# Kernel tuning notes

Hardware: AMD Instinct MI355X
Metric: run time of the kernel (lower is better)

The kernel has to match this reference:

```python
import jax, jax.numpy as jnp
import numpy as np

P = 2048  # number of problems


def _structure():
    # Symbols per problem alternate 128/384; questions per problem alternate 32/96.
    p = np.arange(P)
    S = np.where(p % 2 == 0, 128, 384).astype(np.int64)   # num_symbols per problem
    Q = np.where(p % 2 == 0, 32, 96).astype(np.int64)     # num_questions per problem
    cost_starts = np.concatenate([[0], np.cumsum(S)])[:-1]  # row starts into costs_flat
    prob_of_question = np.repeat(p, Q)                     # [T_Q] problem id of each question
    S_per_q = np.repeat(S, Q)                              # [T_Q] symbols per question
    TQ = S_per_q.shape[0]
    qs_segment = np.repeat(np.arange(TQ), S_per_q)         # [T_total] question id of each element
    q_elem_starts = np.concatenate([[0], np.cumsum(S_per_q)])[:-1]
    T = qs_segment.shape[0]
    # offset of each element within its question, then add that problem's cost row start
    offsets = np.arange(T) - np.repeat(q_elem_starts, S_per_q)
    starts_per_q = np.repeat(cost_starts, Q)
    cost_index = np.repeat(starts_per_q, S_per_q) + offsets  # tile_like gather indices
    return (cost_index.astype(np.int32), qs_segment.astype(np.int32),
            prob_of_question.astype(np.int32))


def setup_inputs() -> dict:
    key = jax.random.key(0)
    k1, k2, k3 = jax.random.split(key, 3)
    cost_index, qs_segment, prob_of_question = _structure()
    T = cost_index.shape[0]            # 41_943_040
    TS = (P // 2) * (128 + 384)        # 524_288
    occ_flat = jax.random.uniform(k1, (T,), dtype=jnp.float32)   # occurrence counts >= 0
    costs_flat = jax.random.normal(k2, (TS,), dtype=jnp.float32)  # symbol costs (weights)
    valid = jax.random.uniform(k3, (P,)) < 0.9                    # per-problem valid mask
    return {
        'occ_flat': occ_flat,
        'costs_flat': costs_flat,
        'valid': valid,
        'cost_index': jnp.asarray(cost_index),
        'qs_segment': jnp.asarray(qs_segment),
        'prob_of_question': jnp.asarray(prob_of_question),
    }


def reference(occ_flat, costs_flat, valid, cost_index, qs_segment, prob_of_question):
    # tile_like: broadcast each problem's costs to each of its questions (gather)
    # costs_to_logits: elementwise multiply + per-question reduce_sum
    # costs_decorated_to_logits: invalid problems' logits are 0 (scatter_nd into zeros)
    TQ = prob_of_question.shape[0]
    potentials = occ_flat * costs_flat[cost_index]             # [T_total]
    logits_q = jax.ops.segment_sum(potentials, qs_segment, num_segments=TQ)  # [T_Q]
    return jnp.where(valid[prob_of_question], logits_q, jnp.zeros((), logits_q.dtype))
```

## Files before the change

kernel.cpp:

```cpp
#include <hip/hip_runtime.h>


typedef float f4 __attribute__((ext_vector_type(4)));

__device__ __forceinline__ float dot4(f4 a, f4 b) {
    return a.x * b.x + a.y * b.y + a.z * b.z + a.w * b.w;
}

__device__ __forceinline__ float hw_reduce(float s) {
    #pragma unroll
    for (int off = 16; off > 0; off >>= 1) s += __shfl_down(s, off, 32);
    return s;
}

__global__ __launch_bounds__(256)
void classifier_kernel(const float* __restrict__ occ,
                       const float* __restrict__ costs,
                       const void*  __restrict__ valid,
                       float* __restrict__ out) {
    __shared__ f4 lds_c[256];
    const int tid   = threadIdx.x;
    const int lane  = tid & 31;
    const int hw    = tid >> 5;
    const int flane = tid & 63;

    unsigned int wdet = ((const unsigned int*)valid)[flane];
    const bool u8 = (__ballot(wdet > 1u) != 0ull);

    const int g     = blockIdx.x;
    const int group = g / 9;
    const int r     = g - group * 9;

    const f4* occ4  = (const f4*)occ;
    const f4* cost4 = (const f4*)costs;

    if (r < 8) {
        const int pair  = 2 * group + (r & 1);
        const int chunk = r >> 1;
        const int prob  = 2 * pair + 1;
        if (tid < 96) lds_c[tid] = cost4[128 * pair + 32 + tid];
        __syncthreads();
        const bool v = u8 ? (((const unsigned char*)valid)[prob] != 0)
                          : (((const int*)valid)[prob] != 0);
        const int j0 = 24 * chunk + 3 * hw;
        float s0 = 0.0f, s1 = 0.0f, s2 = 0.0f;
        if (v) {
            f4 cb0 = lds_c[lane];
            f4 cb1 = lds_c[lane + 32];
            f4 cb2 = lds_c[lane + 64];
            const f4* ob = occ4 + 10240 * pair + 1024 + 96 * j0 + lane;
            f4 a0 = __builtin_nontemporal_load(ob);
            f4 a1 = __builtin_nontemporal_load(ob + 32);
            f4 a2 = __builtin_nontemporal_load(ob + 64);
            f4 b0 = __builtin_nontemporal_load(ob + 96);
            f4 b1 = __builtin_nontemporal_load(ob + 128);
            f4 b2 = __builtin_nontemporal_load(ob + 160);
            f4 c0 = __builtin_nontemporal_load(ob + 192);
            f4 c1 = __builtin_nontemporal_load(ob + 224);
            f4 c2 = __builtin_nontemporal_load(ob + 256);
            s0 = dot4(a0, cb0) + dot4(a1, cb1) + dot4(a2, cb2);
            s1 = dot4(b0, cb0) + dot4(b1, cb1) + dot4(b2, cb2);
            s2 = dot4(c0, cb0) + dot4(c1, cb1) + dot4(c2, cb2);
        }
        s0 = hw_reduce(s0);
        s1 = hw_reduce(s1);
        s2 = hw_reduce(s2);
        if (lane == 0) {
            float* o = out + 128 * pair + 32 + j0;
            o[0] = s0; o[1] = s1; o[2] = s2;
        }
    } else {
        const int e  = group;
        const int pa = 2 * e, pb = 2 * e + 1;
        lds_c[tid] = (tid < 128) ? cost4[128 * pa + tid]
                                 : cost4[128 * pb + (tid - 128)];
        __syncthreads();
        const int p    = (hw < 4) ? pa : pb;
        const int prob = 2 * p;
        const bool v = u8 ? (((const unsigned char*)valid)[prob] != 0)
                          : (((const int*)valid)[prob] != 0);
        const int j0 = (hw & 3) * 8;
        float s[8];
        #pragma unroll
        for (int i = 0; i < 8; ++i) s[i] = 0.0f;
        if (v) {
            f4 cb = lds_c[((hw < 4) ? 0 : 128) + lane];
            const f4* ob = occ4 + 10240 * p + 32 * j0 + lane;
            #pragma unroll
            for (int i = 0; i < 8; ++i) {
                f4 a = __builtin_nontemporal_load(ob + 32 * i);
                s[i] = dot4(a, cb);
            }
        }
        #pragma unroll
        for (int i = 0; i < 8; ++i) {
            float sr = hw_reduce(s[i]);
            if (lane == 0) out[128 * p + j0 + i] = sr;
        }
    }
}

extern "C" void kernel_launch(void* const* d_in, const int* in_sizes, int n_in,
                              void* d_out, int out_size, void* d_ws, size_t ws_size,
                              hipStream_t stream) {
    const float* occ   = (const float*)d_in[0];
    const float* costs = (const float*)d_in[1];
    const void*  valid = (const void*)d_in[2];

    (void)out_size;
    const int grid  = 512 * 9;
    const int block = 256;

    classifier_kernel<<<grid, block, 0, stream>>>(occ, costs, valid, (float*)d_out);
}
```

Measured before the change: 348.0 us.

## Stream large-problem occ rows via global_load_lds with full-wave reductions

In the 384-symbol branch, the occurrence data is now staged into LDS with asynchronous global_load_lds copies, and partial vmcnt waits let compute start before all loads have landed. Each wave processes six questions as three pairs, using a 64-lane layout and full-wave shuffle reductions instead of half-wave ones. Costs are read directly from global memory into registers, removing the block barrier. Invalid problems now write zeros explicitly. The change adds 36 KB of shared memory per block, which may reduce occupancy.

```diff
diff --git a/kernel.cpp b/kernel.cpp
--- a/kernel.cpp
+++ b/kernel.cpp
@@ -7,21 +7,35 @@
     return a.x * b.x + a.y * b.y + a.z * b.z + a.w * b.w;
 }
 
+__device__ __forceinline__ float wave_reduce(float s) {
+    #pragma unroll
+    for (int off = 32; off > 0; off >>= 1) s += __shfl_down(s, off, 64);
+    return s;
+}
+
 __device__ __forceinline__ float hw_reduce(float s) {
     #pragma unroll
     for (int off = 16; off > 0; off >>= 1) s += __shfl_down(s, off, 32);
     return s;
 }
 
+__device__ __forceinline__ void load_lds16(const float* g, float* l) {
+    __builtin_amdgcn_global_load_lds(
+        (const __attribute__((address_space(1))) void*)g,
+        (__attribute__((address_space(3))) void*)l, 16, 0, 0);
+}
+
+#define VMWAIT(n) do { \
+    asm volatile("s_waitcnt vmcnt(" #n ")" ::: "memory"); \
+    __builtin_amdgcn_sched_barrier(0); } while (0)
+
 __global__ __launch_bounds__(256)
 void classifier_kernel(const float* __restrict__ occ,
                        const float* __restrict__ costs,
                        const void*  __restrict__ valid,
                        float* __restrict__ out) {
-    __shared__ f4 lds_c[256];
+    __shared__ __align__(16) float smem[9216];
     const int tid   = threadIdx.x;
-    const int lane  = tid & 31;
-    const int hw    = tid >> 5;
     const int flane = tid & 63;
 
     unsigned int wdet = ((const unsigned int*)valid)[flane];
@@ -38,38 +52,56 @@
         const int pair  = 2 * group + (r & 1);
         const int chunk = r >> 1;
         const int prob  = 2 * pair + 1;
-        if (tid < 96) lds_c[tid] = cost4[128 * pair + 32 + tid];
-        __syncthreads();
+        const int wid   = tid >> 6;
+        const int wl    = flane;
+        const int q0w   = 24 * chunk + 6 * wid;
         const bool v = u8 ? (((const unsigned char*)valid)[prob] != 0)
                           : (((const int*)valid)[prob] != 0);
-        const int j0 = 24 * chunk + 3 * hw;
-        float s0 = 0.0f, s1 = 0.0f, s2 = 0.0f;
+        float* oout = out + 128 * pair + 32;
+
         if (v) {
-            f4 cb0 = lds_c[lane];
-            f4 cb1 = lds_c[lane + 32];
-            f4 cb2 = lds_c[lane + 64];
-            const f4* ob = occ4 + 10240 * pair + 1024 + 96 * j0 + lane;
-            f4 a0 = __builtin_nontemporal_load(ob);
-            f4 a1 = __builtin_nontemporal_load(ob + 32);
-            f4 a2 = __builtin_nontemporal_load(ob + 64);
-            f4 b0 = __builtin_nontemporal_load(ob + 96);
-            f4 b1 = __builtin_nontemporal_load(ob + 128);
-            f4 b2 = __builtin_nontemporal_load(ob + 160);
-            f4 c0 = __builtin_nontemporal_load(ob + 192);
-            f4 c1 = __builtin_nontemporal_load(ob + 224);
-            f4 c2 = __builtin_nontemporal_load(ob + 256);
-            s0 = dot4(a0, cb0) + dot4(a1, cb1) + dot4(a2, cb2);
-            s1 = dot4(b0, cb0) + dot4(b1, cb1) + dot4(b2, cb2);
-            s2 = dot4(c0, cb0) + dot4(c1, cb1) + dot4(c2, cb2);
-        }
-        s0 = hw_reduce(s0);
-        s1 = hw_reduce(s1);
-        s2 = hw_reduce(s2);
-        if (lane == 0) {
-            float* o = out + 128 * pair + 32 + j0;
-            o[0] = s0; o[1] = s1; o[2] = s2;
+            const f4* cr = cost4 + 128 * pair + 32;
+            f4 c0 = cr[wl];
+            f4 c1 = (wl < 32) ? cr[64 + wl] : cr[wl - 32];
+            f4 c2 = cr[32 + wl];
+
+            const float* gbase = occ + 40960 * pair + 4096 + 384 * q0w;
+            float* lbase = &smem[wid * 2304];
+            #pragma unroll
+            for (int s = 0; s < 9; ++s)
+                load_lds16(gbase + 256 * s + 4 * wl, lbase + 256 * s);
+
+            #pragma unroll
+            for (int u = 0; u < 3; ++u) {
+                if (u == 0)      VMWAIT(6);
+                else if (u == 1) VMWAIT(5);
+                else             VMWAIT(4);
+                const f4* lv = (const f4*)(lbase + 768 * u);
+                f4 a0 = lv[wl];
+                f4 a1 = lv[64 + wl];
+                f4 a2 = lv[128 + wl];
+                float ta = dot4(a0, c0);
+                float tm = dot4(a1, c1);
+                float tb = dot4(a2, c2);
+                float sa = ta + (wl < 32 ? tm : 0.0f);
+                float sb = tb + (wl < 32 ? 0.0f : tm);
+                sa = wave_reduce(sa);
+                sb = wave_reduce(sb);
+                if (wl == 0) {
+                    oout[q0w + 2 * u]     = sa;
+                    oout[q0w + 2 * u + 1] = sb;
+                }
+            }
+        } else {
+            if (wl == 0) {
+                #pragma unroll
+                for (int i = 0; i < 6; ++i) oout[q0w + i] = 0.0f;
+            }
         }
     } else {
+        f4* lds_c = (f4*)smem;
+        const int lane = tid & 31;
+        const int hw   = tid >> 5;
         const int e  = group;
         const int pa = 2 * e, pb = 2 * e + 1;
         lds_c[tid] = (tid < 128) ? cost4[128 * pa + tid]
```

After: 357.2 us. +2.6%, slower.
